# Kernel optimization log

Measured on AMD Instinct MI355X. Metric: run time of the kernel, lower is better.

The kernel has to match this reference:

```python
import jax, jax.numpy as jnp
import numpy as np

B, T, H, L, NB, NL = 32, 512, 256, 2048, 256, 4
F0_MIN, F0_MAX = 0.0, 1.0
E_MIN, E_MAX = 0.0, 1.0


def setup_inputs() -> dict:
    key = jax.random.key(0)
    ks = jax.random.split(key, 12)
    s = 1.0 / np.sqrt(H)
    return {
        "x": jax.random.normal(ks[0], (B, T, H), jnp.float32),
        "src_seq": jax.random.uniform(ks[1], (B, T, 3), jnp.float32, 1.0, 8.0),
        "duration_target": jax.random.randint(ks[2], (B, T), 0, 7, jnp.int32),
        "pitch_target": jax.random.uniform(ks[3], (B, L), jnp.float32),
        "energy_target": jax.random.uniform(ks[4], (B, L), jnp.float32),
        "src_mask": jnp.zeros((B, T), bool),
        "max_len": L,
        "dur_W": jax.random.normal(ks[5], (NL, H, H), jnp.float32) * s,
        "dur_b": jnp.zeros((NL, H), jnp.float32),
        "dur_w": jax.random.normal(ks[6], (H,), jnp.float32) * s,
        "dur_b2": jnp.zeros((1,), jnp.float32),
        "pit_W": jax.random.normal(ks[7], (NL, H, H), jnp.float32) * s,
        "pit_b": jnp.zeros((NL, H), jnp.float32),
        "pit_w": jax.random.normal(ks[8], (H,), jnp.float32) * s,
        "pit_b2": jnp.zeros((1,), jnp.float32),
        "en_W": jax.random.normal(ks[9], (NL, H, H), jnp.float32) * s,
        "en_b": jnp.zeros((NL, H), jnp.float32),
        "en_w": jax.random.normal(ks[10], (H,), jnp.float32) * s,
        "en_b2": jnp.zeros((1,), jnp.float32),
        "pitch_emb": jax.random.normal(ks[11], (2 * NB, H), jnp.float32),
        "energy_emb": jax.random.normal(jax.random.fold_in(key, 99), (2 * NB, H), jnp.float32),
    }


def _predictor(h, W, b, w, b2, mask):
    # stand-in for Decoder(n_layers=4) + Linear(H, 1) head
    for i in range(NL):
        h = jax.nn.relu(jnp.einsum('blh,hk->blk', h, W[i]) + b[i])
    out = jnp.einsum('blh,h->bl', h, w) + b2[0]
    return jnp.where(mask, 0.0, out)


def _length_regulate(x, dur, max_len):
    # cumsum-based repeat_interleave: frame m maps to token searchsorted(cumsum(dur), m, 'right')
    cum = jnp.cumsum(dur, axis=1)                      # [B, T]
    mel_len = jnp.minimum(cum[:, -1], max_len)         # [B]
    frames = jnp.arange(max_len)                       # [L]
    idx = jax.vmap(lambda c: jnp.searchsorted(c, frames, side='right'))(cum)
    idx = jnp.clip(idx, 0, x.shape[1] - 1)             # [B, L]
    out = jnp.take_along_axis(x, idx[:, :, None], axis=1)  # [B, L, H]
    mel_mask = frames[None, :] >= mel_len[:, None]     # True = padding
    out = out * (~mel_mask)[:, :, None]
    return out, mel_len, mel_mask


def reference(x, src_seq, duration_target, pitch_target, energy_target, src_mask, max_len,
              dur_W, dur_b, dur_w, dur_b2, pit_W, pit_b, pit_w, pit_b2,
              en_W, en_b, en_w, en_b2, pitch_emb, energy_emb):
    # duration predictor: LengthPredictor = decoder + linear + tanh, scaled by note lengths
    d = _predictor(x, dur_W, dur_b, dur_w, dur_b2, src_mask)
    log_duration_prediction = (jnp.tanh(d) + 1.0) * src_seq[:, :, 2]

    # length regulator (training path: duration_target provided)
    xe, mel_len, mel_mask = _length_regulate(x, duration_target, max_len)

    pitch_prediction = jax.nn.relu(_predictor(xe, pit_W, pit_b, pit_w, pit_b2, mel_mask))
    p_idx = jnp.ceil((pitch_target - F0_MIN) / (F0_MAX - F0_MIN) * NB).astype(jnp.int32)
    p_emb = pitch_emb[p_idx]                            # [B, L, H]

    energy_prediction = _predictor(xe, en_W, en_b, en_w, en_b2, mel_mask)
    e_idx = jnp.ceil((energy_target - E_MIN) / (E_MAX - E_MIN) * NB).astype(jnp.int32)
    e_emb = energy_emb[e_idx]                           # [B, L, H]

    out = xe + p_emb + e_emb
    return out, log_duration_prediction, pitch_prediction, energy_prediction, mel_len, mel_mask
```

## Files before the change

kernel.cpp:

```cpp
#include <hip/hip_runtime.h>

typedef _Float16 half_t;
typedef _Float16 half4 __attribute__((ext_vector_type(4)));
typedef _Float16 half8 __attribute__((ext_vector_type(8)));
typedef float floatx4 __attribute__((ext_vector_type(4)));

#define HST 264
#define B_ 32
#define T_ 512
#define H_ 256
#define L_ 2048

__global__ void prep_weights_kernel(const float* __restrict__ dur_W,
                                    const float* __restrict__ pit_W,
                                    const float* __restrict__ en_W,
                                    half_t* __restrict__ Wp) {
  int g = blockIdx.x * 256 + threadIdx.x;
  int lane = g & 63;
  int t = g >> 6;
  int nt = t & 15;
  int kk = (t >> 4) & 7;
  int layer = (t >> 7) & 3;
  int pred = t >> 9;
  const float* W = (pred == 0 ? dur_W : (pred == 1 ? pit_W : en_W)) + layer * 65536;
  int n = nt * 16 + (lane & 15);
  int k0 = kk * 32 + (lane >> 4) * 8;
  half8 o;
#pragma unroll
  for (int j = 0; j < 8; ++j) o[j] = (half_t)W[(k0 + j) * 256 + n];
  *(half8*)&Wp[(size_t)t * 512 + lane * 8] = o;
}

__global__ void meta_kernel(const int* __restrict__ dur,
                            const float* __restrict__ pitch_t,
                            const float* __restrict__ energy_t,
                            int* __restrict__ idx_ws,
                            int* __restrict__ pi_ws,
                            int* __restrict__ ei_ws,
                            int* __restrict__ ml_ws,
                            float* __restrict__ out4,
                            float* __restrict__ out5) {
  __shared__ int cum_l[T_];
  __shared__ int ml_s;
  int b = blockIdx.x >> 2;
  int chunk = blockIdx.x & 3;
  int tid = threadIdx.x;
  if (tid < 64) {
    int l = tid;
    const int* dr = dur + b * T_;
    int v[8];
    int base = l * 8;
#pragma unroll
    for (int j = 0; j < 8; ++j) v[j] = dr[base + j];
#pragma unroll
    for (int j = 1; j < 8; ++j) v[j] += v[j - 1];
    int tot = v[7];
    int inc = tot;
    for (int d = 1; d < 64; d <<= 1) {
      int t = __shfl_up(inc, d);
      if (l >= d) inc += t;
    }
    int excl = inc - tot;
#pragma unroll
    for (int j = 0; j < 8; ++j) cum_l[base + j] = excl + v[j];
    if (l == 63) {
      int mel = min(inc, L_);
      ml_s = mel;
      if (chunk == 0) {
        ml_ws[b] = mel;
        out4[b] = (float)mel;
      }
    }
  }
  __syncthreads();
  int ml = ml_s;
#pragma unroll
  for (int j = 0; j < 2; ++j) {
    int m = chunk * 512 + j * 256 + tid;
    int lo = 0;
#pragma unroll
    for (int sh = 8; sh >= 0; --sh) {
      int c = lo + (1 << sh);
      if (c <= T_ && cum_l[c - 1] <= m) lo = c;
    }
    int idx = min(lo, T_ - 1);
    int g = b * L_ + m;
    idx_ws[g] = idx;
    pi_ws[g] = (int)ceilf(pitch_t[g] * 256.0f);
    ei_ws[g] = (int)ceilf(energy_t[g] * 256.0f);
    out5[g] = (m >= ml) ? 1.0f : 0.0f;
  }
}

__global__ void out0_kernel(const float* __restrict__ x,
                            const float* __restrict__ pemb,
                            const float* __restrict__ eemb,
                            const int* __restrict__ idx_ws,
                            const int* __restrict__ pi_ws,
                            const int* __restrict__ ei_ws,
                            const int* __restrict__ ml_ws,
                            float* __restrict__ out0) {
  int wid = blockIdx.x * 4 + (threadIdx.x >> 6);
  int lane = threadIdx.x & 63;
  int b = wid >> 11;
  int m = wid & (L_ - 1);
  int ml = ml_ws[b];
  int ir = idx_ws[wid];
  int pi = pi_ws[wid];
  int ei = ei_ws[wid];
  float4 xv = {0.f, 0.f, 0.f, 0.f};
  if (m < ml) xv = *(const float4*)&x[((size_t)(b * T_ + ir)) * H_ + lane * 4];
  const float4 pv = *(const float4*)&pemb[(size_t)pi * H_ + lane * 4];
  const float4 ev = *(const float4*)&eemb[(size_t)ei * H_ + lane * 4];
  float4 o;
  o.x = xv.x + pv.x + ev.x;
  o.y = xv.y + pv.y + ev.y;
  o.z = xv.z + pv.z + ev.z;
  o.w = xv.w + pv.w + ev.w;
  *(float4*)&out0[(size_t)wid * H_ + lane * 4] = o;
}

__global__ __launch_bounds__(128) void predictor_kernel(
    const float* __restrict__ x,
    const half_t* __restrict__ Wp,
    const float* __restrict__ dur_b, const float* __restrict__ dur_w, const float* __restrict__ dur_b2,
    const float* __restrict__ pit_b, const float* __restrict__ pit_w, const float* __restrict__ pit_b2,
    const float* __restrict__ en_b,  const float* __restrict__ en_w,  const float* __restrict__ en_b2,
    const int* __restrict__ idx_ws, const int* __restrict__ mlw,
    const float* __restrict__ src_seq, const unsigned char* __restrict__ src_mask,
    float* __restrict__ out1, float* __restrict__ out2, float* __restrict__ out3) {
  __shared__ half_t hlds[64 * HST];
  int bid = blockIdx.x;
  int mode, blk;
  const half_t* W; const float* bias; const float* wh; const float* b2p; float* outp;
  if (bid < 1024)      { mode = 1; blk = bid;        W = Wp + 262144; bias = pit_b; wh = pit_w; b2p = pit_b2; outp = out2; }
  else if (bid < 2048) { mode = 2; blk = bid - 1024; W = Wp + 524288; bias = en_b;  wh = en_w;  b2p = en_b2;  outp = out3; }
  else                 { mode = 0; blk = bid - 2048; W = Wp;          bias = dur_b; wh = dur_w; b2p = dur_b2; outp = out1; }

  int tid = threadIdx.x;
  int wv = tid >> 6, lane = tid & 63;
  int mi = lane & 15, qi = lane >> 4;
  int wrow0 = wv * 32;
  int brow0 = blk * 64;

  if (mode == 0) {
    for (int it = 0; it < 32; ++it) {
      int rl = wrow0 + it;
      const float4 xv = *(const float4*)&x[(size_t)(brow0 + rl) * H_ + lane * 4];
      half4 h4;
      h4[0] = (half_t)xv.x; h4[1] = (half_t)xv.y;
      h4[2] = (half_t)xv.z; h4[3] = (half_t)xv.w;
      *(half4*)&hlds[rl * HST + lane * 4] = h4;
    }
  } else {
    int b = brow0 >> 11;
    int m0 = brow0 & (L_ - 1);
    int ml = mlw[b];
    for (int it = 0; it < 32; ++it) {
      int rl = wrow0 + it;
      int m = m0 + rl;
      float4 xv = {0.f, 0.f, 0.f, 0.f};
      if (m < ml) {
        int ir = idx_ws[b * L_ + m];
        xv = *(const float4*)&x[((size_t)(b * T_ + ir)) * H_ + lane * 4];
      }
      half4 h4;
      h4[0] = (half_t)xv.x; h4[1] = (half_t)xv.y;
      h4[2] = (half_t)xv.z; h4[3] = (half_t)xv.w;
      *(half4*)&hlds[rl * HST + lane * 4] = h4;
    }
  }

#pragma unroll 1
  for (int layer = 0; layer < 4; ++layer) {
    half8 hf[2][8];
#pragma unroll
    for (int mt = 0; mt < 2; ++mt)
#pragma unroll
      for (int kk = 0; kk < 8; ++kk)
        hf[mt][kk] = *(const half8*)&hlds[(wrow0 + mt * 16 + mi) * HST + kk * 32 + qi * 8];

    const half_t* wl = W + (size_t)layer * 65536;
    const float* bl = bias + layer * 256;
    half8 wA[8], wB[8];
    float4 bA, bB;
#pragma unroll
    for (int kk = 0; kk < 8; ++kk)
      wA[kk] = *(const half8*)&wl[(size_t)(kk * 16 + 0) * 512 + lane * 8];
    bA = *(const float4*)&bl[0 * 16 + qi * 4];

#pragma unroll
    for (int ntp = 0; ntp < 8; ++ntp) {
      int nt0 = ntp * 2;
#pragma unroll
      for (int kk = 0; kk < 8; ++kk)
        wB[kk] = *(const half8*)&wl[(size_t)(kk * 16 + nt0 + 1) * 512 + lane * 8];
      bB = *(const float4*)&bl[(nt0 + 1) * 16 + qi * 4];
      {
        floatx4 acc0 = {bA.x, bA.y, bA.z, bA.w};
        floatx4 acc1 = {bA.x, bA.y, bA.z, bA.w};
#pragma unroll
        for (int kk = 0; kk < 8; ++kk) {
          acc0 = __builtin_amdgcn_mfma_f32_16x16x32_f16(wA[kk], hf[0][kk], acc0, 0, 0, 0);
          acc1 = __builtin_amdgcn_mfma_f32_16x16x32_f16(wA[kk], hf[1][kk], acc1, 0, 0, 0);
        }
        int colbase = nt0 * 16 + qi * 4;
        half4 h40, h41;
        h40[0] = (half_t)fmaxf(acc0[0], 0.f); h40[1] = (half_t)fmaxf(acc0[1], 0.f);
        h40[2] = (half_t)fmaxf(acc0[2], 0.f); h40[3] = (half_t)fmaxf(acc0[3], 0.f);
        h41[0] = (half_t)fmaxf(acc1[0], 0.f); h41[1] = (half_t)fmaxf(acc1[1], 0.f);
        h41[2] = (half_t)fmaxf(acc1[2], 0.f); h41[3] = (half_t)fmaxf(acc1[3], 0.f);
        *(half4*)&hlds[(wrow0 + mi) * HST + colbase] = h40;
        *(half4*)&hlds[(wrow0 + 16 + mi) * HST + colbase] = h41;
      }
      if (ntp < 7) {
#pragma unroll
        for (int kk = 0; kk < 8; ++kk)
          wA[kk] = *(const half8*)&wl[(size_t)(kk * 16 + nt0 + 2) * 512 + lane * 8];
        bA = *(const float4*)&bl[(nt0 + 2) * 16 + qi * 4];
      }
      {
        floatx4 acc0 = {bB.x, bB.y, bB.z, bB.w};
        floatx4 acc1 = {bB.x, bB.y, bB.z, bB.w};
#pragma unroll
        for (int kk = 0; kk < 8; ++kk) {
          acc0 = __builtin_amdgcn_mfma_f32_16x16x32_f16(wB[kk], hf[0][kk], acc0, 0, 0, 0);
          acc1 = __builtin_amdgcn_mfma_f32_16x16x32_f16(wB[kk], hf[1][kk], acc1, 0, 0, 0);
        }
        int colbase = (nt0 + 1) * 16 + qi * 4;
        half4 h40, h41;
        h40[0] = (half_t)fmaxf(acc0[0], 0.f); h40[1] = (half_t)fmaxf(acc0[1], 0.f);
        h40[2] = (half_t)fmaxf(acc0[2], 0.f); h40[3] = (half_t)fmaxf(acc0[3], 0.f);
        h41[0] = (half_t)fmaxf(acc1[0], 0.f); h41[1] = (half_t)fmaxf(acc1[1], 0.f);
        h41[2] = (half_t)fmaxf(acc1[2], 0.f); h41[3] = (half_t)fmaxf(acc1[3], 0.f);
        *(half4*)&hlds[(wrow0 + mi) * HST + colbase] = h40;
        *(half4*)&hlds[(wrow0 + 16 + mi) * HST + colbase] = h41;
      }
    }
  }

  {
    int r = lane >> 1, hf2 = lane & 1;
    int rl = wrow0 + r;
    float sum = 0.f;
    const half_t* hrow = &hlds[rl * HST + hf2 * 128];
    const float* whp = wh + hf2 * 128;
#pragma unroll
    for (int j = 0; j < 16; ++j) {
      half8 hv = *(const half8*)&hrow[j * 8];
#pragma unroll
      for (int u = 0; u < 8; ++u) sum += (float)hv[u] * whp[j * 8 + u];
    }
    sum += __shfl_xor(sum, 1);
    if (hf2 == 0) {
      int row = brow0 + rl;
      float d = sum + b2p[0];
      if (mode == 0) {
        if (src_mask[row]) d = 0.f;
        float s2 = src_seq[(size_t)row * 3 + 2];
        outp[row] = (tanhf(d) + 1.0f) * s2;
      } else {
        int b = row >> 11;
        int m = row & (L_ - 1);
        float v = (m >= mlw[b]) ? 0.f : d;
        outp[row] = (mode == 1) ? fmaxf(v, 0.f) : v;
      }
    }
  }
}

extern "C" void kernel_launch(void* const* d_in, const int* in_sizes, int n_in,
                              void* d_out, int out_size, void* d_ws, size_t ws_size,
                              hipStream_t stream) {
  const float* x        = (const float*)d_in[0];
  const float* src_seq  = (const float*)d_in[1];
  const int*   durt     = (const int*)d_in[2];
  const float* pitcht   = (const float*)d_in[3];
  const float* energyt  = (const float*)d_in[4];
  const unsigned char* src_mask = (const unsigned char*)d_in[5];
  const float* dur_W  = (const float*)d_in[7];
  const float* dur_b  = (const float*)d_in[8];
  const float* dur_w  = (const float*)d_in[9];
  const float* dur_b2 = (const float*)d_in[10];
  const float* pit_W  = (const float*)d_in[11];
  const float* pit_b  = (const float*)d_in[12];
  const float* pit_w  = (const float*)d_in[13];
  const float* pit_b2 = (const float*)d_in[14];
  const float* en_W   = (const float*)d_in[15];
  const float* en_b   = (const float*)d_in[16];
  const float* en_w   = (const float*)d_in[17];
  const float* en_b2  = (const float*)d_in[18];
  const float* pemb   = (const float*)d_in[19];
  const float* eemb   = (const float*)d_in[20];

  float* out0 = (float*)d_out;
  float* out1 = out0 + 16777216;
  float* out2 = out1 + 16384;
  float* out3 = out2 + 65536;
  float* out4 = out3 + 65536;
  float* out5 = out4 + 32;

  int* idx_ws = (int*)d_ws;
  int* pi_ws  = idx_ws + 65536;
  int* ei_ws  = pi_ws + 65536;
  int* ml_ws  = ei_ws + 65536;
  half_t* Wp  = (half_t*)((char*)d_ws + 786560);

  prep_weights_kernel<<<dim3(384), dim3(256), 0, stream>>>(dur_W, pit_W, en_W, Wp);
  meta_kernel<<<dim3(128), dim3(256), 0, stream>>>(durt, pitcht, energyt,
                                                   idx_ws, pi_ws, ei_ws, ml_ws, out4, out5);
  out0_kernel<<<dim3(16384), dim3(256), 0, stream>>>(x, pemb, eemb,
                                                     idx_ws, pi_ws, ei_ws, ml_ws, out0);
  predictor_kernel<<<dim3(2304), dim3(128), 0, stream>>>(
      x, Wp,
      dur_b, dur_w, dur_b2,
      pit_b, pit_w, pit_b2,
      en_b, en_w, en_b2,
      idx_ws, ml_ws, src_seq, src_mask,
      out1, out2, out3);
}
```

Baseline: 249.1 us.

## Fuse out0 gather into predictor, merge setup kernels, split N across waves

Merges weight preparation and metadata computation into one setup kernel, and folds the out0 gather-add (x + pitch/energy embeddings) into the pitch predictor's activation load so the x rows are gathered once and out0 is written with nontemporal stores. The predictor now has each wave cover all 64 rows but half of the output columns, which halves per-wave weight fetches and needs block-wide barriers around the LDS activation updates. Weight prefetch now runs across layer boundaries. The cost is higher register pressure (hf[4][8] fragments plus two weight sets) and extra syncthreads per layer.

```diff
diff --git a/kernel.cpp b/kernel.cpp
--- a/kernel.cpp
+++ b/kernel.cpp
@@ -11,40 +11,45 @@
 #define H_ 256
 #define L_ 2048
 
-__global__ void prep_weights_kernel(const float* __restrict__ dur_W,
-                                    const float* __restrict__ pit_W,
-                                    const float* __restrict__ en_W,
-                                    half_t* __restrict__ Wp) {
-  int g = blockIdx.x * 256 + threadIdx.x;
-  int lane = g & 63;
-  int t = g >> 6;
-  int nt = t & 15;
-  int kk = (t >> 4) & 7;
-  int layer = (t >> 7) & 3;
-  int pred = t >> 9;
-  const float* W = (pred == 0 ? dur_W : (pred == 1 ? pit_W : en_W)) + layer * 65536;
-  int n = nt * 16 + (lane & 15);
-  int k0 = kk * 32 + (lane >> 4) * 8;
-  half8 o;
-#pragma unroll
-  for (int j = 0; j < 8; ++j) o[j] = (half_t)W[(k0 + j) * 256 + n];
-  *(half8*)&Wp[(size_t)t * 512 + lane * 8] = o;
-}
-
-__global__ void meta_kernel(const int* __restrict__ dur,
-                            const float* __restrict__ pitch_t,
-                            const float* __restrict__ energy_t,
-                            int* __restrict__ idx_ws,
-                            int* __restrict__ pi_ws,
-                            int* __restrict__ ei_ws,
-                            int* __restrict__ ml_ws,
-                            float* __restrict__ out4,
-                            float* __restrict__ out5) {
+__global__ __launch_bounds__(256) void setup_kernel(
+    const int* __restrict__ dur,
+    const float* __restrict__ pitch_t,
+    const float* __restrict__ energy_t,
+    const float* __restrict__ dur_W,
+    const float* __restrict__ pit_W,
+    const float* __restrict__ en_W,
+    half_t* __restrict__ Wp,
+    int* __restrict__ idx_ws,
+    int* __restrict__ pi_ws,
+    int* __restrict__ ei_ws,
+    int* __restrict__ ml_ws,
+    float* __restrict__ out4,
+    float* __restrict__ out5) {
   __shared__ int cum_l[T_];
   __shared__ int ml_s;
-  int b = blockIdx.x >> 2;
-  int chunk = blockIdx.x & 3;
+  int bid = blockIdx.x;
   int tid = threadIdx.x;
+
+  if (bid >= 128) {
+    int g = (bid - 128) * 256 + tid;
+    int lane = g & 63;
+    int t = g >> 6;
+    int nt = t & 15;
+    int kk = (t >> 4) & 7;
+    int layer = (t >> 7) & 3;
+    int pred = t >> 9;
+    const float* W = (pred == 0 ? dur_W : (pred == 1 ? pit_W : en_W)) + layer * 65536;
+    int n = nt * 16 + (lane & 15);
+    int k0 = kk * 32 + (lane >> 4) * 8;
+    half8 o;
+#pragma unroll
+    for (int j = 0; j < 8; ++j) o[j] = (half_t)W[(k0 + j) * 256 + n];
+    *(half8*)&Wp[(size_t)t * 512 + lane * 8] = o;
+    return;
+  }
+
+  int b = bid >> 2;
+  int chunk = bid & 3;
   if (tid < 64) {
     int l = tid;
     const int* dr = dur + b * T_;
@@ -92,43 +97,45 @@
   }
 }
 
-__global__ void out0_kernel(const float* __restrict__ x,
-                            const float* __restrict__ pemb,
-                            const float* __restrict__ eemb,
-                            const int* __restrict__ idx_ws,
-                            const int* __restrict__ pi_ws,
-                            const int* __restrict__ ei_ws,
-                            const int* __restrict__ ml_ws,
-                            float* __restrict__ out0) {
-  int wid = blockIdx.x * 4 + (threadIdx.x >> 6);
-  int lane = threadIdx.x & 63;
-  int b = wid >> 11;
-  int m = wid & (L_ - 1);
-  int ml = ml_ws[b];
-  int ir = idx_ws[wid];
-  int pi = pi_ws[wid];
-  int ei = ei_ws[wid];
-  float4 xv = {0.f, 0.f, 0.f, 0.f};
-  if (m < ml) xv = *(const float4*)&x[((size_t)(b * T_ + ir)) * H_ + lane * 4];
-  const float4 pv = *(const float4*)&pemb[(size_t)pi * H_ + lane * 4];
-  const float4 ev = *(const float4*)&eemb[(size_t)ei * H_ + lane * 4];
-  float4 o;
-  o.x = xv.x + pv.x + ev.x;
-  o.y = xv.y + pv.y + ev.y;
-  o.z = xv.z + pv.z + ev.z;
-  o.w = xv.w + pv.w + ev.w;
-  *(float4*)&out0[(size_t)wid * H_ + lane * 4] = o;
-}
-
-__global__ __launch_bounds__(128) void predictor_kernel(
+#define CHUNK(WREG, BREG, NT)                                                      \
+  {                                                                                \
+    floatx4 a0 = {BREG.x, BREG.y, BREG.z, BREG.w};                                 \
+    floatx4 a1 = a0, a2 = a0, a3 = a0;                                             \
+    _Pragma("unroll")                                                              \
+    for (int kk = 0; kk < 8; ++kk) {                                               \
+      a0 = __builtin_amdgcn_mfma_f32_16x16x32_f16(WREG[kk], hf[0][kk], a0, 0, 0, 0); \
+      a1 = __builtin_amdgcn_mfma_f32_16x16x32_f16(WREG[kk], hf[1][kk], a1, 0, 0, 0); \
+      a2 = __builtin_amdgcn_mfma_f32_16x16x32_f16(WREG[kk], hf[2][kk], a2, 0, 0, 0); \
+      a3 = __builtin_amdgcn_mfma_f32_16x16x32_f16(WREG[kk], hf[3][kk], a3, 0, 0, 0); \
+    }                                                                              \
+    int colbase = (NT) * 16 + qi * 4;                                              \
+    half4 hw0, hw1, hw2, hw3;                                                      \
+    hw0[0] = (half_t)fmaxf(a0[0], 0.f); hw0[1] = (half_t)fmaxf(a0[1], 0.f);        \
+    hw0[2] = (half_t)fmaxf(a0[2], 0.f); hw0[3] = (half_t)fmaxf(a0[3], 0.f);        \
+    hw1[0] = (half_t)fmaxf(a1[0], 0.f); hw1[1] = (half_t)fmaxf(a1[1], 0.f);        \
+    hw1[2] = (half_t)fmaxf(a1[2], 0.f); hw1[3] = (half_t)fmaxf(a1[3], 0.f);        \
+    hw2[0] = (half_t)fmaxf(a2[0], 0.f); hw2[1] = (half_t)fmaxf(a2[1], 0.f);        \
+    hw2[2] = (half_t)fmaxf(a2[2], 0.f); hw2[3] = (half_t)fmaxf(a2[3], 0.f);        \
+    hw3[0] = (half_t)fmaxf(a3[0], 0.f); hw3[1] = (half_t)fmaxf(a3[1], 0.f);        \
+    hw3[2] = (half_t)fmaxf(a3[2], 0.f); hw3[3] = (half_t)fmaxf(a3[3], 0.f);        \
+    *(half4*)&hlds[(0 * 16 + mi) * HST + colbase] = hw0;                           \
+    *(half4*)&hlds[(1 * 16 + mi) * HST + colbase] = hw1;                           \
+    *(half4*)&hlds[(2 * 16 + mi) * HST + colbase] = hw2;                           \
+    *(half4*)&hlds[(3 * 16 + mi) * HST + colbase] = hw3;                           \
+  }
+
+__global__ __launch_bounds__(128, 2) void predictor_kernel(
     const float* __restrict__ x,
     const half_t* __restrict__ Wp,
     const float* __restrict__ dur_b, const float* __restrict__ dur_w, const float* __restrict__ dur_b2,
     const float* __restrict__ pit_b, const float* __restrict__ pit_w, const float* __restrict__ pit_b2,
     const float* __restrict__ en_b,  const float* __restrict__ en_w,  const float* __restrict__ en_b2,
-    const int* __restrict__ idx_ws, const int* __restrict__ mlw,
+    const int* __restrict__ idx_ws, const int* __restrict__ pi_ws, const int* __restrict__ ei_ws,
+    const int* __restrict__ mlw,
     const float* __restrict__ src_seq, const unsigned char* __restrict__ src_mask,
-    float* __restrict__ out1, float* __restrict__ out2, float* __restrict__ out3) {
+    const float* __restrict__ pemb, const float* __restrict__ eemb,
+    float* __restrict__ out0, float* __restrict__ out1,
+    float* __restrict__ out2, float* __restrict__ out3) {
   __shared__ half_t hlds[64 * HST];
   int bid = blockIdx.x;
   int mode, blk;
@@ -140,12 +147,12 @@
   int tid = threadIdx.x;
   int wv = tid >> 6, lane = tid & 63;
   int mi = lane & 15, qi = lane >> 4;
-  int wrow0 = wv * 32;
+  int srow0 = wv * 32;
   int brow0 = blk * 64;
 
   if (mode == 0) {
     for (int it = 0; it < 32; ++it) {
-      int rl = wrow0 + it;
+      int rl = srow0 + it;
       const float4 xv = *(const float4*)&x[(size_t)(brow0 + rl) * H_ + lane * 4];
       half4 h4;
       h4[0] = (half_t)xv.x; h4[1] = (half_t)xv.y;
@@ -157,12 +164,23 @@
     int m0 = brow0 & (L_ - 1);
     int ml = mlw[b];
     for (int it = 0; it < 32; ++it) {
-      int rl = wrow0 + it;
+      int rl = srow0 + it;
       int m = m0 + rl;
+      int g = b * L_ + m;
       float4 xv = {0.f, 0.f, 0.f, 0.f};
       if (m < ml) {
-        int ir = idx_ws[b * L_ + m];
+        int ir = idx_ws[g];
         xv = *(const float4*)&x[((size_t)(b * T_ + ir)) * H_ + lane * 4];
+      }
+      if (mode == 1) {
+        const float4 pv = *(const float4*)&pemb[(size_t)pi_ws[g] * H_ + lane * 4];
+        const float4 ev = *(const float4*)&eemb[(size_t)ei_ws[g] * H_ + lane * 4];
+        floatx4 o;
+        o[0] = xv.x + pv.x + ev.x;
+        o[1] = xv.y + pv.y + ev.y;
+        o[2] = xv.z + pv.z + ev.z;
+        o[3] = xv.w + pv.w + ev.w;
+        __builtin_nontemporal_store(o, (floatx4*)&out0[(size_t)g * H_ + lane * 4]);
       }
       half4 h4;
       h4[0] = (half_t)xv.x; h4[1] = (half_t)xv.y;
@@ -170,78 +188,56 @@
       *(half4*)&hlds[rl * HST + lane * 4] = h4;
     }
   }
+  __syncthreads();
+
+  int nt0 = wv * 8;
+  half8 wA[8], wB[8];
+  float4 bA, bB;
+#pragma unroll
+  for (int kk = 0; kk < 8; ++kk)
+    wA[kk] = *(const half8*)&W[(size_t)(kk * 16 + nt0) * 512 + lane * 8];
+  bA = *(const float4*)&bias[nt0 * 16 + qi * 4];
 
 #pragma unroll 1
   for (int layer = 0; layer < 4; ++layer) {
-    half8 hf[2][8];
-#pragma unroll
-    for (int mt = 0; mt < 2; ++mt)
-#pragma unroll
-      for (int kk = 0; kk < 8; ++kk)
-        hf[mt][kk] = *(const half8*)&hlds[(wrow0 + mt * 16 + mi) * HST + kk * 32 + qi * 8];
-
     const half_t* wl = W + (size_t)layer * 65536;
     const float* bl = bias + layer * 256;
-    half8 wA[8], wB[8];
-    float4 bA, bB;
-#pragma unroll
-    for (int kk = 0; kk < 8; ++kk)
-      wA[kk] = *(const half8*)&wl[(size_t)(kk * 16 + 0) * 512 + lane * 8];
-    bA = *(const float4*)&bl[0 * 16 + qi * 4];
-
-#pragma unroll
-    for (int ntp = 0; ntp < 8; ++ntp) {
-      int nt0 = ntp * 2;
+
+    half8 hf[4][8];
+#pragma unroll
+    for (int mt = 0; mt < 4; ++mt)
 #pragma unroll
       for (int kk = 0; kk < 8; ++kk)
-        wB[kk] = *(const half8*)&wl[(size_t)(kk * 16 + nt0 + 1) * 512 + lane * 8];
-      bB = *(const float4*)&bl[(nt0 + 1) * 16 + qi * 4];
-      {
-        floatx4 acc0 = {bA.x, bA.y, bA.z, bA.w};
-        floatx4 acc1 = {bA.x, bA.y, bA.z, bA.w};
-#pragma unroll
-        for (int kk = 0; kk < 8; ++kk) {
-          acc0 = __builtin_amdgcn_mfma_f32_16x16x32_f16(wA[kk], hf[0][kk], acc0, 0, 0, 0);
-          acc1 = __builtin_amdgcn_mfma_f32_16x16x32_f16(wA[kk], hf[1][kk], acc1, 0, 0, 0);
-        }
-        int colbase = nt0 * 16 + qi * 4;
-        half4 h40, h41;
-        h40[0] = (half_t)fmaxf(acc0[0], 0.f); h40[1] = (half_t)fmaxf(acc0[1], 0.f);
-        h40[2] = (half_t)fmaxf(acc0[2], 0.f); h40[3] = (half_t)fmaxf(acc0[3], 0.f);
-        h41[0] = (half_t)fmaxf(acc1[0], 0.f); h41[1] = (half_t)fmaxf(acc1[1], 0.f);
-        h41[2] = (half_t)fmaxf(acc1[2], 0.f); h41[3] = (half_t)fmaxf(acc1[3], 0.f);
-        *(half4*)&hlds[(wrow0 + mi) * HST + colbase] = h40;
-        *(half4*)&hlds[(wrow0 + 16 + mi) * HST + colbase] = h41;
-      }
-      if (ntp < 7) {
+        hf[mt][kk] = *(const half8*)&hlds[(mt * 16 + mi) * HST + kk * 32 + qi * 8];
+    __syncthreads();
+
+#pragma unroll
+    for (int ntp = 0; ntp < 4; ++ntp) {
+      int ntA = nt0 + ntp * 2;
+#pragma unroll
+      for (int kk = 0; kk < 8; ++kk)
+        wB[kk] = *(const half8*)&wl[(size_t)(kk * 16 + ntA + 1) * 512 + lane * 8];
+      bB = *(const float4*)&bl[(ntA + 1) * 16 + qi * 4];
+      CHUNK(wA, bA, ntA);
+      if (ntp < 3) {
 #pragma unroll
         for (int kk = 0; kk < 8; ++kk)
-          wA[kk] = *(const half8*)&wl[(size_t)(kk * 16 + nt0 + 2) * 512 + lane * 8];
-        bA = *(const float4*)&bl[(nt0 + 2) * 16 + qi * 4];
-      }
-      {
-        floatx4 acc0 = {bB.x, bB.y, bB.z, bB.w};
-        floatx4 acc1 = {bB.x, bB.y, bB.z, bB.w};
-#pragma unroll
-        for (int kk = 0; kk < 8; ++kk) {
-          acc0 = __builtin_amdgcn_mfma_f32_16x16x32_f16(wB[kk], hf[0][kk], acc0, 0, 0, 0);
-          acc1 = __builtin_amdgcn_mfma_f32_16x16x32_f16(wB[kk], hf[1][kk], acc1, 0, 0, 0);
-        }
-        int colbase = (nt0 + 1) * 16 + qi * 4;
-        half4 h40, h41;
-        h40[0] = (half_t)fmaxf(acc0[0], 0.f); h40[1] = (half_t)fmaxf(acc0[1], 0.f);
-        h40[2] = (half_t)fmaxf(acc0[2], 0.f); h40[3] = (half_t)fmaxf(acc0[3], 0.f);
-        h41[0] = (half_t)fmaxf(acc1[0], 0.f); h41[1] = (half_t)fmaxf(acc1[1], 0.f);
-        h41[2] = (half_t)fmaxf(acc1[2], 0.f); h41[3] = (half_t)fmaxf(acc1[3], 0.f);
-        *(half4*)&hlds[(wrow0 + mi) * HST + colbase] = h40;
-        *(half4*)&hlds[(wrow0 + 16 + mi) * HST + colbase] = h41;
-      }
-    }
+          wA[kk] = *(const half8*)&wl[(size_t)(kk * 16 + ntA + 2) * 512 + lane * 8];
+        bA = *(const float4*)&bl[(ntA + 2) * 16 + qi * 4];
+      } else if (layer < 3) {
+#pragma unroll
+        for (int kk = 0; kk < 8; ++kk)
+          wA[kk] = *(const half8*)&wl[(size_t)(65536 + (kk * 16 + nt0) * 512) + lane * 8];
+        bA = *(const float4*)&bl[256 + nt0 * 16 + qi * 4];
+      }
+      CHUNK(wB, bB, ntA + 1);
+    }
+    __syncthreads();
   }
 
   {
     int r = lane >> 1, hf2 = lane & 1;
-    int rl = wrow0 + r;
+    int rl = srow0 + r;
     float sum = 0.f;
     const half_t* hrow = &hlds[rl * HST + hf2 * 128];
     const float* whp = wh + hf2 * 128;
@@ -306,16 +302,14 @@
   int* ml_ws  = ei_ws + 65536;
   half_t* Wp  = (half_t*)((char*)d_ws + 786560);
 
-  prep_weights_kernel<<<dim3(384), dim3(256), 0, stream>>>(dur_W, pit_W, en_W, Wp);
-  meta_kernel<<<dim3(128), dim3(256), 0, stream>>>(durt, pitcht, energyt,
-                                                   idx_ws, pi_ws, ei_ws, ml_ws, out4, out5);
-  out0_kernel<<<dim3(16384), dim3(256), 0, stream>>>(x, pemb, eemb,
-                                                     idx_ws, pi_ws, ei_ws, ml_ws, out0);
+  setup_kernel<<<dim3(512), dim3(256), 0, stream>>>(
+      durt, pitcht, energyt, dur_W, pit_W, en_W, Wp,
+      idx_ws, pi_ws, ei_ws, ml_ws, out4, out5);
   predictor_kernel<<<dim3(2304), dim3(128), 0, stream>>>(
       x, Wp,
       dur_b, dur_w, dur_b2,
       pit_b, pit_w, pit_b2,
       en_b, en_w, en_b2,
-      idx_ws, ml_ws, src_seq, src_mask,
-      out1, out2, out3);
+      idx_ws, pi_ws, ei_ws, ml_ws, src_seq, src_mask, pemb, eemb,
+      out0, out1, out2, out3);
 }
```

Result: slower. 268.3 us (+7.7%).

## Fuse out0 embedding-add into predictor gather and merge setup kernels

Applied to the files above, without the earlier changes.

Merges the weight-prep and metadata kernels into one launch with block-range dispatch. Removes the separate out0 kernel and has pitch-predictor blocks write the final xe+pitch_emb+energy_emb output while they already gather the expanded x rows, using nontemporal stores. This saves two launches and a second gather of x, at the cost of extra loads and stores inside the predictor's gather phase, which may unbalance pitch blocks against energy blocks.

```diff
diff --git a/kernel.cpp b/kernel.cpp
--- a/kernel.cpp
+++ b/kernel.cpp
@@ -11,40 +11,45 @@
 #define H_ 256
 #define L_ 2048
 
-__global__ void prep_weights_kernel(const float* __restrict__ dur_W,
-                                    const float* __restrict__ pit_W,
-                                    const float* __restrict__ en_W,
-                                    half_t* __restrict__ Wp) {
-  int g = blockIdx.x * 256 + threadIdx.x;
-  int lane = g & 63;
-  int t = g >> 6;
-  int nt = t & 15;
-  int kk = (t >> 4) & 7;
-  int layer = (t >> 7) & 3;
-  int pred = t >> 9;
-  const float* W = (pred == 0 ? dur_W : (pred == 1 ? pit_W : en_W)) + layer * 65536;
-  int n = nt * 16 + (lane & 15);
-  int k0 = kk * 32 + (lane >> 4) * 8;
-  half8 o;
-#pragma unroll
-  for (int j = 0; j < 8; ++j) o[j] = (half_t)W[(k0 + j) * 256 + n];
-  *(half8*)&Wp[(size_t)t * 512 + lane * 8] = o;
-}
-
-__global__ void meta_kernel(const int* __restrict__ dur,
-                            const float* __restrict__ pitch_t,
-                            const float* __restrict__ energy_t,
-                            int* __restrict__ idx_ws,
-                            int* __restrict__ pi_ws,
-                            int* __restrict__ ei_ws,
-                            int* __restrict__ ml_ws,
-                            float* __restrict__ out4,
-                            float* __restrict__ out5) {
+__global__ __launch_bounds__(256) void setup_kernel(
+    const int* __restrict__ dur,
+    const float* __restrict__ pitch_t,
+    const float* __restrict__ energy_t,
+    const float* __restrict__ dur_W,
+    const float* __restrict__ pit_W,
+    const float* __restrict__ en_W,
+    half_t* __restrict__ Wp,
+    int* __restrict__ idx_ws,
+    int* __restrict__ pi_ws,
+    int* __restrict__ ei_ws,
+    int* __restrict__ ml_ws,
+    float* __restrict__ out4,
+    float* __restrict__ out5) {
   __shared__ int cum_l[T_];
   __shared__ int ml_s;
-  int b = blockIdx.x >> 2;
-  int chunk = blockIdx.x & 3;
+  int bid = blockIdx.x;
   int tid = threadIdx.x;
+
+  if (bid >= 128) {
+    int g = (bid - 128) * 256 + tid;
+    int lane = g & 63;
+    int t = g >> 6;
+    int nt = t & 15;
+    int kk = (t >> 4) & 7;
+    int layer = (t >> 7) & 3;
+    int pred = t >> 9;
+    const float* W = (pred == 0 ? dur_W : (pred == 1 ? pit_W : en_W)) + layer * 65536;
+    int n = nt * 16 + (lane & 15);
+    int k0 = kk * 32 + (lane >> 4) * 8;
+    half8 o;
+#pragma unroll
+    for (int j = 0; j < 8; ++j) o[j] = (half_t)W[(k0 + j) * 256 + n];
+    *(half8*)&Wp[(size_t)t * 512 + lane * 8] = o;
+    return;
+  }
+
+  int b = bid >> 2;
+  int chunk = bid & 3;
   if (tid < 64) {
     int l = tid;
     const int* dr = dur + b * T_;
@@ -92,43 +97,18 @@
   }
 }
 
-__global__ void out0_kernel(const float* __restrict__ x,
-                            const float* __restrict__ pemb,
-                            const float* __restrict__ eemb,
-                            const int* __restrict__ idx_ws,
-                            const int* __restrict__ pi_ws,
-                            const int* __restrict__ ei_ws,
-                            const int* __restrict__ ml_ws,
-                            float* __restrict__ out0) {
-  int wid = blockIdx.x * 4 + (threadIdx.x >> 6);
-  int lane = threadIdx.x & 63;
-  int b = wid >> 11;
-  int m = wid & (L_ - 1);
-  int ml = ml_ws[b];
-  int ir = idx_ws[wid];
-  int pi = pi_ws[wid];
-  int ei = ei_ws[wid];
-  float4 xv = {0.f, 0.f, 0.f, 0.f};
-  if (m < ml) xv = *(const float4*)&x[((size_t)(b * T_ + ir)) * H_ + lane * 4];
-  const float4 pv = *(const float4*)&pemb[(size_t)pi * H_ + lane * 4];
-  const float4 ev = *(const float4*)&eemb[(size_t)ei * H_ + lane * 4];
-  float4 o;
-  o.x = xv.x + pv.x + ev.x;
-  o.y = xv.y + pv.y + ev.y;
-  o.z = xv.z + pv.z + ev.z;
-  o.w = xv.w + pv.w + ev.w;
-  *(float4*)&out0[(size_t)wid * H_ + lane * 4] = o;
-}
-
 __global__ __launch_bounds__(128) void predictor_kernel(
     const float* __restrict__ x,
     const half_t* __restrict__ Wp,
     const float* __restrict__ dur_b, const float* __restrict__ dur_w, const float* __restrict__ dur_b2,
     const float* __restrict__ pit_b, const float* __restrict__ pit_w, const float* __restrict__ pit_b2,
     const float* __restrict__ en_b,  const float* __restrict__ en_w,  const float* __restrict__ en_b2,
-    const int* __restrict__ idx_ws, const int* __restrict__ mlw,
+    const int* __restrict__ idx_ws, const int* __restrict__ pi_ws, const int* __restrict__ ei_ws,
+    const int* __restrict__ mlw,
     const float* __restrict__ src_seq, const unsigned char* __restrict__ src_mask,
-    float* __restrict__ out1, float* __restrict__ out2, float* __restrict__ out3) {
+    const float* __restrict__ pemb, const float* __restrict__ eemb,
+    float* __restrict__ out0, float* __restrict__ out1,
+    float* __restrict__ out2, float* __restrict__ out3) {
   __shared__ half_t hlds[64 * HST];
   int bid = blockIdx.x;
   int mode, blk;
@@ -159,10 +139,21 @@
     for (int it = 0; it < 32; ++it) {
       int rl = wrow0 + it;
       int m = m0 + rl;
+      int g = b * L_ + m;
       float4 xv = {0.f, 0.f, 0.f, 0.f};
       if (m < ml) {
-        int ir = idx_ws[b * L_ + m];
+        int ir = idx_ws[g];
         xv = *(const float4*)&x[((size_t)(b * T_ + ir)) * H_ + lane * 4];
+      }
+      if (mode == 1) {
+        const float4 pv = *(const float4*)&pemb[(size_t)pi_ws[g] * H_ + lane * 4];
+        const float4 ev = *(const float4*)&eemb[(size_t)ei_ws[g] * H_ + lane * 4];
+        floatx4 o;
+        o[0] = xv.x + pv.x + ev.x;
+        o[1] = xv.y + pv.y + ev.y;
+        o[2] = xv.z + pv.z + ev.z;
+        o[3] = xv.w + pv.w + ev.w;
+        __builtin_nontemporal_store(o, (floatx4*)&out0[(size_t)g * H_ + lane * 4]);
       }
       half4 h4;
       h4[0] = (half_t)xv.x; h4[1] = (half_t)xv.y;
@@ -306,16 +297,14 @@
   int* ml_ws  = ei_ws + 65536;
   half_t* Wp  = (half_t*)((char*)d_ws + 786560);
 
-  prep_weights_kernel<<<dim3(384), dim3(256), 0, stream>>>(dur_W, pit_W, en_W, Wp);
-  meta_kernel<<<dim3(128), dim3(256), 0, stream>>>(durt, pitcht, energyt,
-                                                   idx_ws, pi_ws, ei_ws, ml_ws, out4, out5);
-  out0_kernel<<<dim3(16384), dim3(256), 0, stream>>>(x, pemb, eemb,
-                                                     idx_ws, pi_ws, ei_ws, ml_ws, out0);
+  setup_kernel<<<dim3(512), dim3(256), 0, stream>>>(
+      durt, pitcht, energyt, dur_W, pit_W, en_W, Wp,
+      idx_ws, pi_ws, ei_ws, ml_ws, out4, out5);
   predictor_kernel<<<dim3(2304), dim3(128), 0, stream>>>(
       x, Wp,
       dur_b, dur_w, dur_b2,
       pit_b, pit_w, pit_b2,
       en_b, en_w, en_b2,
-      idx_ws, ml_ws, src_seq, src_mask,
-      out1, out2, out3);
+      idx_ws, pi_ws, ei_ws, ml_ws, src_seq, src_mask, pemb, eemb,
+      out0, out1, out2, out3);
 }
```

Result: no change. 245.2 us (-1.6%).
